# Kernel optimization log

Hardware: AMD Instinct MI355X
Metric: run time of the kernel (lower is better)

Reference implementation:

```python
import jax, jax.numpy as jnp
import numpy as np

K = 3
STRIDE = 1
PAD = 1
GROUPS = 16
EPS = 1e-5


def _conv2d(x, w, b, stride, pad):
    out = jax.lax.conv_general_dilated(
        x, w, (stride, stride), [(pad, pad), (pad, pad)],
        dimension_numbers=("NCHW", "OIHW", "NCHW"))
    return out + b[None, :, None, None]


def setup_inputs() -> dict:
    key = jax.random.key(0)
    ks = jax.random.split(key, 6)
    B, Cin, H, W = 4, 256, 64, 64
    Cout = 256
    x = jax.random.normal(ks[0], (B, Cin, H, W), dtype=jnp.float32)
    # DCNv2 offset/mask-generating conv: 3*K*K = 27 output channels
    w_off = jax.random.normal(ks[1], (3 * K * K, Cin, K, K), dtype=jnp.float32) * 0.01
    b_off = jnp.zeros((3 * K * K,), dtype=jnp.float32)
    # main deformable conv weight/bias
    weight = jax.random.normal(ks[2], (Cout, Cin, K, K), dtype=jnp.float32) * 0.02
    bias = jnp.zeros((Cout,), dtype=jnp.float32)
    # GroupNorm affine params
    gamma = jnp.ones((Cout,), dtype=jnp.float32)
    beta = jnp.zeros((Cout,), dtype=jnp.float32)
    return {"x": x, "w_off": w_off, "b_off": b_off,
            "weight": weight, "bias": bias, "gamma": gamma, "beta": beta}


def reference(x, w_off, b_off, weight, bias, gamma, beta):
    B, Cin, H, W = x.shape
    Cout = weight.shape[0]
    KK = K * K

    # --- offset/mask branch (DCNv2): 18 offsets + 9 sigmoid masks ---
    om = _conv2d(x, w_off, b_off, STRIDE, PAD)          # [B, 27, Ho, Wo]
    Ho, Wo = om.shape[2], om.shape[3]
    off_y, off_x, m = jnp.split(om, 3, axis=1)          # each [B, 9, Ho, Wo]
    mask = jax.nn.sigmoid(m)

    # --- sampling coordinates: base grid + kernel tap + learned offset ---
    kgy = jnp.repeat(jnp.arange(K, dtype=x.dtype), K)   # [9] row of tap
    kgx = jnp.tile(jnp.arange(K, dtype=x.dtype), K)     # [9] col of tap
    base_y = jnp.arange(Ho, dtype=x.dtype) * STRIDE - PAD
    base_x = jnp.arange(Wo, dtype=x.dtype) * STRIDE - PAD
    py = base_y[None, None, :, None] + kgy[None, :, None, None] + off_y  # [B,9,Ho,Wo]
    px = base_x[None, None, None, :] + kgx[None, :, None, None] + off_x  # [B,9,Ho,Wo]

    # --- bilinear sampling with zero padding outside the image ---
    y0 = jnp.floor(py)
    x0 = jnp.floor(px)
    wy1 = py - y0
    wx1 = px - x0

    def gather(img, yy, xx):
        # img [Cin,H,W], yy/xx [9,Ho,Wo] int -> [Cin,9,Ho,Wo]
        return img[:, yy, xx]

    def corner(yi, xi, wy, wx):
        valid = (yi >= 0) & (yi < H) & (xi >= 0) & (xi < W)
        yc = jnp.clip(yi, 0, H - 1).astype(jnp.int32)
        xc = jnp.clip(xi, 0, W - 1).astype(jnp.int32)
        vals = jax.vmap(gather)(x, yc, xc)               # [B,Cin,9,Ho,Wo]
        w_ = (wy * wx * valid.astype(x.dtype))[:, None]   # [B,1,9,Ho,Wo]
        return vals * w_

    sampled = (corner(y0, x0, (1 - wy1), (1 - wx1))
               + corner(y0, x0 + 1, (1 - wy1), wx1)
               + corner(y0 + 1, x0, wy1, (1 - wx1))
               + corner(y0 + 1, x0 + 1, wy1, wx1))       # [B,Cin,9,Ho,Wo]
    sampled = sampled * mask[:, None]                     # modulation

    # --- conv accumulation over taps and input channels ---
    out = jnp.einsum("bckhw,ock->bohw", sampled,
                     weight.reshape(Cout, Cin, KK)) + bias[None, :, None, None]

    # --- GroupNorm(16, Cout) ---
    og = out.reshape(B, GROUPS, Cout // GROUPS, Ho, Wo)
    mu = og.mean(axis=(2, 3, 4), keepdims=True)
    var = og.var(axis=(2, 3, 4), keepdims=True)
    og = (og - mu) * jax.lax.rsqrt(var + EPS)
    out = og.reshape(B, Cout, Ho, Wo) * gamma[None, :, None, None] + beta[None, :, None, None]
    return out
```

## Files before the change

kernel.cpp:

```cpp
#include <hip/hip_runtime.h>
#include <math.h>

#define CIN   256
#define COUT  256
#define H     64
#define W     64
#define HW    4096
#define KK    9
#define KC    2304
#define NOFF  27
#define B_    4
#define EPS   1e-5f
#define OM3S  (B_ * NOFF * HW)

typedef __attribute__((ext_vector_type(4))) float f32x4;
typedef __attribute__((ext_vector_type(8))) short s16x8;

static __device__ __forceinline__ unsigned short f2bf(float f) {
  unsigned u = __builtin_bit_cast(unsigned, f);
  u += 0x7FFF + ((u >> 16) & 1);
  return (unsigned short)(u >> 16);
}
static __device__ __forceinline__ float bflo(unsigned u) {
  return __builtin_bit_cast(float, u << 16);
}
static __device__ __forceinline__ float bfhi(unsigned u) {
  return __builtin_bit_cast(float, u & 0xffff0000u);
}
static __device__ __forceinline__ unsigned packbf(float lo, float hi) {
  unsigned ul = __builtin_bit_cast(unsigned, lo);
  unsigned uh = __builtin_bit_cast(unsigned, hi);
  ul += 0x7FFF + ((ul >> 16) & 1);
  uh += 0x7FFF + ((uh >> 16) & 1);
  return (ul >> 16) | (uh & 0xffff0000u);
}
static __device__ __forceinline__ void gl2lds16(const void* g, void* l) {
  __builtin_amdgcn_global_load_lds(
      (const __attribute__((address_space(1))) unsigned int*)g,
      (__attribute__((address_space(3))) unsigned int*)l, 16, 0, 0);
}

__global__ __launch_bounds__(256) void prep_kernel(
    const float* __restrict__ x, const float* __restrict__ w,
    const float* __restrict__ w_off, unsigned short* __restrict__ xT,
    unsigned short* __restrict__ wBf, unsigned short* __restrict__ wOBf,
    float* __restrict__ gstat) {
  int bi = blockIdx.x;
  int t = threadIdx.x;
  if (bi < 256) {
    __shared__ unsigned short tile[64][272];
    int b = bi >> 6, y = bi & 63;
    const float* src = x + (size_t)b * CIN * HW + y * W;
    for (int r = 0; r < 64; ++r) {
      int idx = r * 256 + t;
      int c = idx >> 6, ww = idx & 63;
      tile[ww][c] = f2bf(src[(size_t)c * HW + ww]);
    }
    __syncthreads();
    unsigned short* dst = xT + ((size_t)(b * 64 + y) * 64) * 256;
    for (int r = 0; r < 8; ++r) {
      int idx = r * 2048 + t * 8;
      int ww = idx >> 8, c = idx & 255;
      *(uint4*)(dst + idx) = *(const uint4*)&tile[ww][c];
    }
  } else if (bi < 544) {
    int pkt = (bi - 256) * 256 + t;
    int lane = pkt & 63;
    int tn = (pkt >> 6) & 15;
    int k2 = pkt >> 10;
    int co = tn * 16 + (lane & 15);
    int kb = k2 * 32 + (lane >> 4) * 8;
    unsigned short v[8];
#pragma unroll
    for (int j = 0; j < 8; ++j) {
      int kk = kb + j;
      int kt = kk >> 8, c = kk & 255;
      v[j] = f2bf(w[(co * 256 + c) * 9 + kt]);
    }
    *(uint4*)&wBf[(size_t)pkt * 8] = *(const uint4*)v;
  } else if (bi < 580) {
    int pkt = (bi - 544) * 256 + t;
    int lane = pkt & 63;
    int tn = (pkt >> 6) & 1;
    int k2 = pkt >> 7;
    int oc = tn * 16 + (lane & 15);
    int kb = k2 * 32 + (lane >> 4) * 8;
    unsigned short v[8];
#pragma unroll
    for (int j = 0; j < 8; ++j) {
      int kk = kb + j;
      int kt = kk >> 8, c = kk & 255;
      v[j] = (oc < NOFF) ? f2bf(w_off[(oc * 256 + c) * 9 + kt]) : (unsigned short)0;
    }
    *(uint4*)&wOBf[(size_t)pkt * 8] = *(const uint4*)v;
  } else {
    if (t < 128) gstat[t] = 0.f;
  }
}

__global__ __launch_bounds__(256) void offconv_mfma_kernel(
    const unsigned short* __restrict__ xT, const unsigned short* __restrict__ wOBf,
    float* __restrict__ om3) {
  int bi = blockIdx.x;
  int ts = bi >> 8;
  int row = bi & 255;
  int b = row >> 6, i = row & 63;
  int t = threadIdx.x, lane = t & 63, wv = t >> 6;
  int lr = lane & 15, lq = lane >> 4;
  int p = wv * 16 + lr;
  const unsigned short* xb = xT + (size_t)b * (HW * 256);
  f32x4 acc[2] = {};

  for (int kc = 0; kc < 3; ++kc) {
    int kt = ts * 3 + kc;
    int ky = kt / 3, kx = kt % 3;
    int yy = i - 1 + ky, xx = p - 1 + kx;
    bool ok = ((unsigned)yy < 64u) && ((unsigned)xx < 64u);
    const unsigned short* ap = xb + ((ok ? yy * 64 + xx : 0) << 8) + lq * 8;
#pragma unroll
    for (int c8 = 0; c8 < 8; ++c8) {
      uint4 av = uint4{0, 0, 0, 0};
      if (ok) av = *(const uint4*)(ap + c8 * 32);
      int k2 = kt * 8 + c8;
      s16x8 a = __builtin_bit_cast(s16x8, av);
      s16x8 b0 = *(const s16x8*)(wOBf + ((((k2 * 2 + 0) << 6) | lane) << 3));
      s16x8 b1 = *(const s16x8*)(wOBf + ((((k2 * 2 + 1) << 6) | lane) << 3));
      acc[0] = __builtin_amdgcn_mfma_f32_16x16x32_bf16(a, b0, acc[0], 0, 0, 0);
      acc[1] = __builtin_amdgcn_mfma_f32_16x16x32_bf16(a, b1, acc[1], 0, 0, 0);
    }
  }
#pragma unroll
  for (int tn = 0; tn < 2; ++tn) {
    int oc = tn * 16 + lr;
    if (oc < NOFF) {
      float* ob = om3 + (size_t)ts * OM3S + ((b * NOFF + oc) << 12) + i * 64 + wv * 16;
#pragma unroll
      for (int r = 0; r < 4; ++r) ob[lq * 4 + r] = acc[tn][r];
    }
  }
}

__global__ __launch_bounds__(256, 2) void sampler_kernel(
    const unsigned short* __restrict__ xT, const float* __restrict__ om3,
    const float* __restrict__ b_off, unsigned short* __restrict__ Aout) {
  __shared__ float tapw[32][KK][4];
  __shared__ int   tapc[32][KK][4];
  int bi = blockIdx.x;
  int b = bi >> 7, i = (bi >> 1) & 63, j0 = (bi & 1) * 32;
  int t = threadIdx.x;
  const unsigned short* xb = xT + (size_t)b * (HW * 256);

  for (int idx = t; idx < 32 * KK; idx += 256) {
    int p = idx / KK, k = idx % KK;
    int pix = i * 64 + j0 + p;
    size_t o = (size_t)(b * NOFF) * HW + pix;
    float offy = om3[o + k * HW] + om3[OM3S + o + k * HW] +
                 om3[2 * OM3S + o + k * HW] + b_off[k];
    float offx = om3[o + (9 + k) * HW] + om3[OM3S + o + (9 + k) * HW] +
                 om3[2 * OM3S + o + (9 + k) * HW] + b_off[9 + k];
    float mval = om3[o + (18 + k) * HW] + om3[OM3S + o + (18 + k) * HW] +
                 om3[2 * OM3S + o + (18 + k) * HW] + b_off[18 + k];
    float mask = 1.f / (1.f + __expf(-mval));
    float py = (float)(i - 1 + k / 3) + offy;
    float px = (float)(j0 + p - 1 + k % 3) + offx;
    float y0f = floorf(py), x0f = floorf(px);
    float wy1 = py - y0f, wx1 = px - x0f;
    int y0 = (int)y0f, x0 = (int)x0f;
    bool y0ok = (unsigned)y0 < 64u, y1ok = (unsigned)(y0 + 1) < 64u;
    bool x0ok = (unsigned)x0 < 64u, x1ok = (unsigned)(x0 + 1) < 64u;
    tapw[p][k][0] = (1.f - wy1) * (1.f - wx1) * mask * (float)(y0ok && x0ok);
    tapw[p][k][1] = (1.f - wy1) * wx1 * mask * (float)(y0ok && x1ok);
    tapw[p][k][2] = wy1 * (1.f - wx1) * mask * (float)(y1ok && x0ok);
    tapw[p][k][3] = wy1 * wx1 * mask * (float)(y1ok && x1ok);
    int y0c = min(max(y0, 0), 63), y1c = min(max(y0 + 1, 0), 63);
    int x0c = min(max(x0, 0), 63), x1c = min(max(x0 + 1, 0), 63);
    tapc[p][k][0] = (y0c * 64 + x0c) * 256;
    tapc[p][k][1] = (x1c - x0c) * 256;
    tapc[p][k][2] = (y1c - y0c) * 64 * 256;
    tapc[p][k][3] = 0;
  }
  __syncthreads();

  int p = t >> 3, s = t & 7;
  int gpix = b * 4096 + i * 64 + j0 + p;
  unsigned short* abase = Aout + (size_t)(gpix >> 6) * 36 * 4096;
  int rowoff = (j0 + p) * 64 + ((s ^ (p & 7)) * 8);

  for (int kt = 0; kt < KK; ++kt) {
    f32x4 tw = *(const f32x4*)&tapw[p][kt][0];
    float w00 = tw[0], w01 = tw[1], w10 = tw[2], w11 = tw[3];
    int4 tc = *(const int4*)&tapc[p][kt][0];
    const unsigned short* c00 = xb + tc.x + s * 8;
    int dx = tc.y, dy = tc.z;
#pragma unroll
    for (int g = 0; g < 4; ++g) {
      int cc = g * 64;
      uint4 v00 = *(const uint4*)(c00 + cc);
      uint4 v01 = *(const uint4*)(c00 + dx + cc);
      uint4 v10 = *(const uint4*)(c00 + dy + cc);
      uint4 v11 = *(const uint4*)(c00 + dy + dx + cc);
      const unsigned* a00 = (const unsigned*)&v00;
      const unsigned* a01 = (const unsigned*)&v01;
      const unsigned* a10 = (const unsigned*)&v10;
      const unsigned* a11 = (const unsigned*)&v11;
      uint4 res;
      unsigned* rr = (unsigned*)&res;
#pragma unroll
      for (int q = 0; q < 4; ++q) {
        float lo = w00 * bflo(a00[q]) + w01 * bflo(a01[q]) +
                   w10 * bflo(a10[q]) + w11 * bflo(a11[q]);
        float hi = w00 * bfhi(a00[q]) + w01 * bfhi(a01[q]) +
                   w10 * bfhi(a10[q]) + w11 * bfhi(a11[q]);
        rr[q] = packbf(lo, hi);
      }
      *(uint4*)(abase + (size_t)(kt * 4 + g) * 4096 + rowoff) = res;
    }
  }
}

__global__ __launch_bounds__(256, 2) void gemm_kernel(
    const unsigned short* __restrict__ A, const unsigned short* __restrict__ wBf,
    const float* __restrict__ bias, unsigned short* __restrict__ cvt,
    float* __restrict__ gstat) {
  __shared__ unsigned short At[4][64 * 64];
  int bi = blockIdx.x;
  int mt = bi & 255;
  int m0 = mt * 64;
  int nh = bi >> 8;
  int t = threadIdx.x, lane = t & 63, wv = t >> 6;
  int lr = lane & 15, lq = lane >> 4;

  const char* Asrc = (const char*)A + (size_t)mt * 36 * 8192 + (wv * 16) * 128 + lane * 16;
  const unsigned short* bb = wBf + ((size_t)((nh * 8 + wv * 2) * 64) + lane) * 8;

  f32x4 acc[4][2] = {};
  s16x8 Bfa[2][2], Bfb[2][2];

#define AISSUE(J)                                                            \
  {                                                                          \
    char* db_ = (char*)At + (((J) & 3) * 8192) + (wv * 16) * 128;            \
    gl2lds16(Asrc + (size_t)(J) * 8192, db_);                                \
    gl2lds16(Asrc + (size_t)(J) * 8192 + 1024, db_ + 1024);                  \
  }

#define BISSUE(J, SLOT)                                                      \
  {                                                                          \
    int k2b_ = (J) * 2;                                                      \
    _Pragma("unroll") for (int kh = 0; kh < 2; ++kh)                         \
      _Pragma("unroll") for (int tn = 0; tn < 2; ++tn)                       \
        SLOT[kh][tn] = *(const s16x8*)(bb + (size_t)(k2b_ + kh) * 8192 + tn * 512); \
  }

#define CONSUME(J, SLOT)                                                     \
  {                                                                          \
    const char* buf_ = (const char*)At + (((J) & 3) * 8192);                 \
    _Pragma("unroll") for (int kh = 0; kh < 2; ++kh) {                       \
      s16x8 af[4];                                                           \
      _Pragma("unroll") for (int tm = 0; tm < 4; ++tm) {                     \
        int r_ = tm * 16 + lr;                                               \
        af[tm] = *(const s16x8*)(buf_ + r_ * 128 + (((kh * 4 + lq) ^ (r_ & 7)) * 16)); \
      }                                                                      \
      __builtin_amdgcn_s_setprio(1);                                         \
      _Pragma("unroll") for (int tm = 0; tm < 4; ++tm)                       \
        _Pragma("unroll") for (int tn = 0; tn < 2; ++tn)                     \
          acc[tm][tn] = __builtin_amdgcn_mfma_f32_16x16x32_bf16(             \
              af[tm], SLOT[kh][tn], acc[tm][tn], 0, 0, 0);                   \
      __builtin_amdgcn_s_setprio(0);                                         \
    }                                                                        \
  }

#define PIPE_ITER(J, DO_A, DO_B, SLOT)                                       \
  {                                                                          \
    __builtin_amdgcn_s_barrier();                                            \
    if (DO_A) AISSUE((J) + 3);                                               \
    __builtin_amdgcn_sched_barrier(0);                                       \
    CONSUME(J, SLOT);                                                        \
    if (DO_B) BISSUE((J) + 2, SLOT);                                         \
    __builtin_amdgcn_sched_barrier(0);                                       \
  }

  AISSUE(0);
  AISSUE(1);
  AISSUE(2);
  __builtin_amdgcn_sched_barrier(0);
  BISSUE(0, Bfa);
  BISSUE(1, Bfb);
  __builtin_amdgcn_sched_barrier(0);
  asm volatile("s_waitcnt vmcnt(12)" ::: "memory");
  __builtin_amdgcn_sched_barrier(0);

#pragma unroll 1
  for (int k = 0; k < 32; k += 4) {
    PIPE_ITER(k + 0, 1, 1, Bfa);
    PIPE_ITER(k + 1, 1, 1, Bfb);
    PIPE_ITER(k + 2, 1, 1, Bfa);
    PIPE_ITER(k + 3, 1, 1, Bfb);
  }
  PIPE_ITER(32, 1, 1, Bfa);
  PIPE_ITER(33, 0, 1, Bfb);
  PIPE_ITER(34, 0, 0, Bfa);
  PIPE_ITER(35, 0, 0, Bfb);

#undef AISSUE
#undef BISSUE
#undef CONSUME
#undef PIPE_ITER

  int b = m0 >> 12;
  int poff = m0 & 4095;
#pragma unroll
  for (int tn = 0; tn < 2; ++tn) {
    int co = nh * 128 + wv * 32 + tn * 16 + lr;
    float bco = bias[co];
    unsigned short* cvb = cvt + (size_t)(b * COUT + co) * HW + poff;
    float s = 0.f, q = 0.f;
#pragma unroll
    for (int tm = 0; tm < 4; ++tm) {
      ushort4 st;
#pragma unroll
      for (int r = 0; r < 4; ++r) {
        float v = acc[tm][tn][r] + bco;
        s += v;
        q += v * v;
        ((unsigned short*)&st)[r] = f2bf(v);
      }
      *(ushort4*)(cvb + tm * 16 + lq * 4) = st;
    }
#pragma unroll
    for (int off = 32; off > 0; off >>= 1) {
      s += __shfl_down(s, off, 64);
      q += __shfl_down(q, off, 64);
    }
    if (lane == 0) {
      int g = co >> 4;
      atomicAdd(&gstat[(b * 16 + g) * 2 + 0], s);
      atomicAdd(&gstat[(b * 16 + g) * 2 + 1], q);
    }
  }
}

__global__ __launch_bounds__(256) void gn_apply_kernel(
    const unsigned short* __restrict__ convout, const float* __restrict__ gstat,
    const float* __restrict__ gamma, const float* __restrict__ beta,
    float* __restrict__ out) {
  int vid = blockIdx.x * 256 + threadIdx.x;
  int e = vid * 8;
  int b = e >> 20;
  int c = (e >> 12) & 255;
  int g = c >> 4;
  float S = gstat[(b * 16 + g) * 2 + 0];
  float Q = gstat[(b * 16 + g) * 2 + 1];
  float mu = S * (1.f / 65536.f);
  float var = Q * (1.f / 65536.f) - mu * mu;
  float rs = rsqrtf(var + EPS);
  float a = rs * gamma[c];
  float bb = beta[c] - mu * a;
  uint4 v = *(const uint4*)(convout + e);
  const unsigned* u = (const unsigned*)&v;
  float4 o0, o1;
  o0.x = bflo(u[0]) * a + bb;  o0.y = bfhi(u[0]) * a + bb;
  o0.z = bflo(u[1]) * a + bb;  o0.w = bfhi(u[1]) * a + bb;
  o1.x = bflo(u[2]) * a + bb;  o1.y = bfhi(u[2]) * a + bb;
  o1.z = bflo(u[3]) * a + bb;  o1.w = bfhi(u[3]) * a + bb;
  *(float4*)(out + e) = o0;
  *(float4*)(out + e + 4) = o1;
}

extern "C" void kernel_launch(void* const* d_in, const int* in_sizes, int n_in,
                              void* d_out, int out_size, void* d_ws, size_t ws_size,
                              hipStream_t stream) {
  const float* x      = (const float*)d_in[0];
  const float* w_off  = (const float*)d_in[1];
  const float* b_off  = (const float*)d_in[2];
  const float* weight = (const float*)d_in[3];
  const float* bias   = (const float*)d_in[4];
  const float* gamma  = (const float*)d_in[5];
  const float* beta   = (const float*)d_in[6];
  float* out = (float*)d_out;

  float* om3 = (float*)d_ws;
  unsigned short* xT   = (unsigned short*)(om3 + (size_t)3 * OM3S);
  unsigned short* cvt  = xT;
  unsigned short* wBf  = xT + (size_t)B_ * HW * 256;
  unsigned short* wOBf = wBf + (size_t)COUT * KC;
  unsigned short* Abuf = wOBf + (size_t)32 * KC;
  float* gstat = (float*)(Abuf + (size_t)B_ * HW * KC);

  prep_kernel<<<dim3(581), dim3(256), 0, stream>>>(x, weight, w_off, xT, wBf, wOBf, gstat);
  offconv_mfma_kernel<<<dim3(768), dim3(256), 0, stream>>>(xT, wOBf, om3);
  sampler_kernel<<<dim3(512), dim3(256), 0, stream>>>(xT, om3, b_off, Abuf);
  gemm_kernel<<<dim3(512), dim3(256), 0, stream>>>(Abuf, wBf, bias, cvt, gstat);
  gn_apply_kernel<<<dim3(2048), dim3(256), 0, stream>>>(cvt, gstat, gamma, beta, out);
}
```

Before: 176.5 us.

## Fuse GroupNorm apply into GEMM via cooperative grid sync

Removes the separate GroupNorm apply kernel. The GEMM now keeps its accumulators in registers, waits at a grid-wide cooperative sync until all group statistics are gathered, then normalizes and writes fp32 output directly. This avoids writing and re-reading the bf16 conv output and saves one launch. It requires all 512 blocks to be co-resident (2 per CU at 256 CUs) and adds a grid barrier cost; if the launch cannot fit, the cooperative launch fails.

```diff
diff --git a/kernel.cpp b/kernel.cpp
--- a/kernel.cpp
+++ b/kernel.cpp
@@ -1,4 +1,5 @@
 #include <hip/hip_runtime.h>
+#include <hip/hip_cooperative_groups.h>
 #include <math.h>
 
 #define CIN   256
@@ -220,8 +221,9 @@
 
 __global__ __launch_bounds__(256, 2) void gemm_kernel(
     const unsigned short* __restrict__ A, const unsigned short* __restrict__ wBf,
-    const float* __restrict__ bias, unsigned short* __restrict__ cvt,
-    float* __restrict__ gstat) {
+    const float* __restrict__ bias, const float* __restrict__ gamma,
+    const float* __restrict__ beta, float* __restrict__ gstat,
+    float* __restrict__ out) {
   __shared__ unsigned short At[4][64 * 64];
   int bi = blockIdx.x;
   int mt = bi & 255;
@@ -312,20 +314,16 @@
   for (int tn = 0; tn < 2; ++tn) {
     int co = nh * 128 + wv * 32 + tn * 16 + lr;
     float bco = bias[co];
-    unsigned short* cvb = cvt + (size_t)(b * COUT + co) * HW + poff;
     float s = 0.f, q = 0.f;
 #pragma unroll
-    for (int tm = 0; tm < 4; ++tm) {
-      ushort4 st;
+    for (int tm = 0; tm < 4; ++tm)
 #pragma unroll
       for (int r = 0; r < 4; ++r) {
         float v = acc[tm][tn][r] + bco;
+        acc[tm][tn][r] = v;
         s += v;
         q += v * v;
-        ((unsigned short*)&st)[r] = f2bf(v);
       }
-      *(ushort4*)(cvb + tm * 16 + lq * 4) = st;
-    }
 #pragma unroll
     for (int off = 32; off > 0; off >>= 1) {
       s += __shfl_down(s, off, 64);
@@ -337,33 +335,31 @@
       atomicAdd(&gstat[(b * 16 + g) * 2 + 1], q);
     }
   }
-}
-
-__global__ __launch_bounds__(256) void gn_apply_kernel(
-    const unsigned short* __restrict__ convout, const float* __restrict__ gstat,
-    const float* __restrict__ gamma, const float* __restrict__ beta,
-    float* __restrict__ out) {
-  int vid = blockIdx.x * 256 + threadIdx.x;
-  int e = vid * 8;
-  int b = e >> 20;
-  int c = (e >> 12) & 255;
-  int g = c >> 4;
-  float S = gstat[(b * 16 + g) * 2 + 0];
-  float Q = gstat[(b * 16 + g) * 2 + 1];
-  float mu = S * (1.f / 65536.f);
-  float var = Q * (1.f / 65536.f) - mu * mu;
-  float rs = rsqrtf(var + EPS);
-  float a = rs * gamma[c];
-  float bb = beta[c] - mu * a;
-  uint4 v = *(const uint4*)(convout + e);
-  const unsigned* u = (const unsigned*)&v;
-  float4 o0, o1;
-  o0.x = bflo(u[0]) * a + bb;  o0.y = bfhi(u[0]) * a + bb;
-  o0.z = bflo(u[1]) * a + bb;  o0.w = bfhi(u[1]) * a + bb;
-  o1.x = bflo(u[2]) * a + bb;  o1.y = bfhi(u[2]) * a + bb;
-  o1.z = bflo(u[3]) * a + bb;  o1.w = bfhi(u[3]) * a + bb;
-  *(float4*)(out + e) = o0;
-  *(float4*)(out + e + 4) = o1;
+
+  cooperative_groups::this_grid().sync();
+
+#pragma unroll
+  for (int tn = 0; tn < 2; ++tn) {
+    int co = nh * 128 + wv * 32 + tn * 16 + lr;
+    int g = co >> 4;
+    float S = gstat[(b * 16 + g) * 2 + 0];
+    float Q = gstat[(b * 16 + g) * 2 + 1];
+    float mu = S * (1.f / 65536.f);
+    float var = Q * (1.f / 65536.f) - mu * mu;
+    float rs = rsqrtf(var + EPS);
+    float a = rs * gamma[co];
+    float bb2 = beta[co] - mu * a;
+    float* ob = out + (size_t)(b * COUT + co) * HW + poff;
+#pragma unroll
+    for (int tm = 0; tm < 4; ++tm) {
+      float4 st;
+      st.x = acc[tm][tn][0] * a + bb2;
+      st.y = acc[tm][tn][1] * a + bb2;
+      st.z = acc[tm][tn][2] * a + bb2;
+      st.w = acc[tm][tn][3] * a + bb2;
+      *(float4*)(ob + tm * 16 + lq * 4) = st;
+    }
+  }
 }
 
 extern "C" void kernel_launch(void* const* d_in, const int* in_sizes, int n_in,
@@ -380,7 +376,6 @@
 
   float* om3 = (float*)d_ws;
   unsigned short* xT   = (unsigned short*)(om3 + (size_t)3 * OM3S);
-  unsigned short* cvt  = xT;
   unsigned short* wBf  = xT + (size_t)B_ * HW * 256;
   unsigned short* wOBf = wBf + (size_t)COUT * KC;
   unsigned short* Abuf = wOBf + (size_t)32 * KC;
@@ -389,6 +384,13 @@
   prep_kernel<<<dim3(581), dim3(256), 0, stream>>>(x, weight, w_off, xT, wBf, wOBf, gstat);
   offconv_mfma_kernel<<<dim3(768), dim3(256), 0, stream>>>(xT, wOBf, om3);
   sampler_kernel<<<dim3(512), dim3(256), 0, stream>>>(xT, om3, b_off, Abuf);
-  gemm_kernel<<<dim3(512), dim3(256), 0, stream>>>(Abuf, wBf, bias, cvt, gstat);
-  gn_apply_kernel<<<dim3(2048), dim3(256), 0, stream>>>(cvt, gstat, gamma, beta, out);
-}
+
+  {
+    const unsigned short* Aarg = Abuf;
+    const unsigned short* wArg = wBf;
+    void* kargs[] = {(void*)&Aarg, (void*)&wArg, (void*)&bias, (void*)&gamma,
+                     (void*)&beta, (void*)&gstat, (void*)&out};
+    hipLaunchCooperativeKernel((void*)gemm_kernel, dim3(512), dim3(256),
+                               kargs, 0, stream);
+  }
+}
```

Result: slower. 241.9 us (+37.0%).

## Stage GEMM A tiles through registers with double-buffered LDS

Applied to the files above, without the earlier changes.

Replaces the direct global-to-LDS async loads and 4-deep LDS ring in the GEMM with ordinary global loads into registers, then explicit LDS stores into a 2-slot LDS buffer. The loop is restructured into a ping-pong schedule with one barrier per k-step, and the manual waitcnt and sched_barrier fences are dropped. This halves LDS use, which may allow more resident blocks, and leaves scheduling to the compiler. In exchange it adds register pressure and extra VGPR-to-LDS store instructions, and it gives up the async global_load_lds path.

```diff
diff --git a/kernel.cpp b/kernel.cpp
--- a/kernel.cpp
+++ b/kernel.cpp
@@ -33,11 +33,6 @@
   ul += 0x7FFF + ((ul >> 16) & 1);
   uh += 0x7FFF + ((uh >> 16) & 1);
   return (ul >> 16) | (uh & 0xffff0000u);
-}
-static __device__ __forceinline__ void gl2lds16(const void* g, void* l) {
-  __builtin_amdgcn_global_load_lds(
-      (const __attribute__((address_space(1))) unsigned int*)g,
-      (__attribute__((address_space(3))) unsigned int*)l, 16, 0, 0);
 }
 
 __global__ __launch_bounds__(256) void prep_kernel(
@@ -222,7 +217,7 @@
     const unsigned short* __restrict__ A, const unsigned short* __restrict__ wBf,
     const float* __restrict__ bias, unsigned short* __restrict__ cvt,
     float* __restrict__ gstat) {
-  __shared__ unsigned short At[4][64 * 64];
+  __shared__ unsigned short At[2][64 * 64];
   int bi = blockIdx.x;
   int mt = bi & 255;
   int m0 = mt * 64;
@@ -230,17 +225,23 @@
   int t = threadIdx.x, lane = t & 63, wv = t >> 6;
   int lr = lane & 15, lq = lane >> 4;
 
-  const char* Asrc = (const char*)A + (size_t)mt * 36 * 8192 + (wv * 16) * 128 + lane * 16;
+  const char* Asrc = (const char*)A + (size_t)mt * 36 * 8192 + wv * 2048 + lane * 16;
   const unsigned short* bb = wBf + ((size_t)((nh * 8 + wv * 2) * 64) + lane) * 8;
 
   f32x4 acc[4][2] = {};
   s16x8 Bfa[2][2], Bfb[2][2];
-
-#define AISSUE(J)                                                            \
+  uint4 sA0[2], sA1[2];
+
+#define ALOAD(J, SLOT)                                                       \
   {                                                                          \
-    char* db_ = (char*)At + (((J) & 3) * 8192) + (wv * 16) * 128;            \
-    gl2lds16(Asrc + (size_t)(J) * 8192, db_);                                \
-    gl2lds16(Asrc + (size_t)(J) * 8192 + 1024, db_ + 1024);                  \
+    SLOT[0] = *(const uint4*)(Asrc + (size_t)(J) * 8192);                    \
+    SLOT[1] = *(const uint4*)(Asrc + (size_t)(J) * 8192 + 1024);             \
+  }
+
+#define AWRITE(BUFI, SLOT)                                                   \
+  {                                                                          \
+    *(uint4*)((char*)At[BUFI] + wv * 2048 + lane * 16) = SLOT[0];            \
+    *(uint4*)((char*)At[BUFI] + wv * 2048 + 1024 + lane * 16) = SLOT[1];     \
   }
 
 #define BISSUE(J, SLOT)                                                      \
@@ -251,9 +252,9 @@
         SLOT[kh][tn] = *(const s16x8*)(bb + (size_t)(k2b_ + kh) * 8192 + tn * 512); \
   }
 
-#define CONSUME(J, SLOT)                                                     \
+#define CONSUME(BUFI, SLOT)                                                  \
   {                                                                          \
-    const char* buf_ = (const char*)At + (((J) & 3) * 8192);                 \
+    const char* buf_ = (const char*)At[BUFI];                                \
     _Pragma("unroll") for (int kh = 0; kh < 2; ++kh) {                       \
       s16x8 af[4];                                                           \
       _Pragma("unroll") for (int tm = 0; tm < 4; ++tm) {                     \
@@ -269,42 +270,32 @@
     }                                                                        \
   }
 
-#define PIPE_ITER(J, DO_A, DO_B, SLOT)                                       \
-  {                                                                          \
-    __builtin_amdgcn_s_barrier();                                            \
-    if (DO_A) AISSUE((J) + 3);                                               \
-    __builtin_amdgcn_sched_barrier(0);                                       \
-    CONSUME(J, SLOT);                                                        \
-    if (DO_B) BISSUE((J) + 2, SLOT);                                         \
-    __builtin_amdgcn_sched_barrier(0);                                       \
-  }
-
-  AISSUE(0);
-  AISSUE(1);
-  AISSUE(2);
-  __builtin_amdgcn_sched_barrier(0);
+  ALOAD(0, sA0);
+  ALOAD(1, sA1);
+  AWRITE(0, sA0);
+  ALOAD(2, sA0);
   BISSUE(0, Bfa);
   BISSUE(1, Bfb);
-  __builtin_amdgcn_sched_barrier(0);
-  asm volatile("s_waitcnt vmcnt(12)" ::: "memory");
-  __builtin_amdgcn_sched_barrier(0);
+  __builtin_amdgcn_s_barrier();
 
 #pragma unroll 1
-  for (int k = 0; k < 32; k += 4) {
-    PIPE_ITER(k + 0, 1, 1, Bfa);
-    PIPE_ITER(k + 1, 1, 1, Bfb);
-    PIPE_ITER(k + 2, 1, 1, Bfa);
-    PIPE_ITER(k + 3, 1, 1, Bfb);
-  }
-  PIPE_ITER(32, 1, 1, Bfa);
-  PIPE_ITER(33, 0, 1, Bfb);
-  PIPE_ITER(34, 0, 0, Bfa);
-  PIPE_ITER(35, 0, 0, Bfb);
-
-#undef AISSUE
+  for (int k = 0; k < 36; k += 2) {
+    CONSUME(0, Bfa);
+    AWRITE(1, sA1);
+    if (k + 3 < 36) ALOAD(k + 3, sA1);
+    if (k + 2 < 36) BISSUE(k + 2, Bfa);
+    __builtin_amdgcn_s_barrier();
+    CONSUME(1, Bfb);
+    if (k + 2 < 36) AWRITE(0, sA0);
+    if (k + 4 < 36) ALOAD(k + 4, sA0);
+    if (k + 3 < 36) BISSUE(k + 3, Bfb);
+    __builtin_amdgcn_s_barrier();
+  }
+
+#undef ALOAD
+#undef AWRITE
 #undef BISSUE
 #undef CONSUME
-#undef PIPE_ITER
 
   int b = m0 >> 12;
   int poff = m0 & 4095;
```

Result: slower. 204.2 us (+15.7%).
